# Performance work log

Measured on AMD Instinct MI355X. Metric: run time of the kernel, lower is better.

Reference implementation:

```python
import jax, jax.numpy as jnp
import numpy as np

T, K, N = 4096, 4096, 11008
EPS = 1e-5


def setup_inputs() -> dict:
    key = jax.random.key(0)
    k1, k2, k3, k4 = jax.random.split(key, 4)
    input_tensor = jax.random.normal(k1, (1, T, K), dtype=jnp.bfloat16)
    # int8 weights in [-127, 127]
    weight = jax.random.randint(k2, (N, K), -127, 128, dtype=jnp.int8)
    # per-output-channel weight scale, small positive values
    weight_scale = (jax.random.uniform(k3, (N, 1), dtype=jnp.float32) * 0.02 + 1e-4)
    bias = jax.random.normal(k4, (N,), dtype=jnp.bfloat16)
    return {"input_tensor": input_tensor, "weight": weight,
            "weight_scale": weight_scale, "bias": bias}


def _quantize_per_token_absmax(x):
    # x: [T, K] float -> int8 quant [T, K], float32 scale [T, 1]
    xf = x.astype(jnp.float32)
    absmax = jnp.max(jnp.abs(xf), axis=-1, keepdims=True)  # [T, 1]
    scale = jnp.maximum(absmax, EPS) / 127.0
    q = jnp.clip(jnp.round(xf / scale), -127, 127).astype(jnp.int8)
    return q, scale


def reference(input_tensor, weight, weight_scale, bias):
    x = jnp.squeeze(input_tensor, axis=0)                  # [T, K]
    x_q, x_scale = _quantize_per_token_absmax(x)           # int8 [T,K], f32 [T,1]
    # int8 GEMM with int32 accumulation: [T, K] @ [K, N]
    acc = jax.lax.dot_general(
        x_q, weight.T,
        dimension_numbers=(((1,), (0,)), ((), ())),
        preferred_element_type=jnp.int32,
    )
    # dequantize: per-token scale * per-channel scale
    out = (acc.astype(jnp.float32) * x_scale * weight_scale.T).astype(jnp.bfloat16)
    out = out + bias
    return out[None, :, :]                                  # [1, T, N]
```

## Files before the change

kernel.cpp:

```cpp
#include <hip/hip_runtime.h>
#include <hip/hip_bf16.h>
#include <stdint.h>

#define T_DIM 4096
#define K_DIM 4096
#define N_DIM 11008

#define XQ_OFF 0
#define XS_OFF 16777216
#define W8_OFF 16793600

typedef __attribute__((ext_vector_type(4))) int v4i;

__global__ __launch_bounds__(256) void prep_kernel(
    const float* __restrict__ x, int8_t* __restrict__ xq, float* __restrict__ xs,
    const int* __restrict__ w32, int8_t* __restrict__ w8)
{
    if (blockIdx.x < T_DIM / 4) {
        const int wid   = threadIdx.x >> 6;
        const int lane  = threadIdx.x & 63;
        const int token = blockIdx.x * 4 + wid;

        const float* xrow = x + (size_t)token * K_DIM;

        float4 v[16];
        float am = 0.0f;
#pragma unroll
        for (int j = 0; j < 16; ++j) {
            v[j] = *(const float4*)(xrow + (size_t)(j * 64 + lane) * 4);
            am = fmaxf(am, fmaxf(fmaxf(fabsf(v[j].x), fabsf(v[j].y)),
                                 fmaxf(fabsf(v[j].z), fabsf(v[j].w))));
        }
#pragma unroll
        for (int m = 1; m < 64; m <<= 1)
            am = fmaxf(am, __shfl_xor(am, m, 64));

        const float scale = fmaxf(am, 1e-5f) / 127.0f;
        if (lane == 0) xs[token] = scale;

        uint32_t* qrow = (uint32_t*)(xq + (size_t)token * K_DIM);
#pragma unroll
        for (int j = 0; j < 16; ++j) {
            int q0 = min(127, max(-127, (int)rintf(v[j].x / scale)));
            int q1 = min(127, max(-127, (int)rintf(v[j].y / scale)));
            int q2 = min(127, max(-127, (int)rintf(v[j].z / scale)));
            int q3 = min(127, max(-127, (int)rintf(v[j].w / scale)));
            qrow[j * 64 + lane] = ((uint32_t)(uint8_t)(int8_t)q0)       |
                                  ((uint32_t)(uint8_t)(int8_t)q1 << 8)  |
                                  ((uint32_t)(uint8_t)(int8_t)q2 << 16) |
                                  ((uint32_t)(uint8_t)(int8_t)q3 << 24);
        }
    } else {
        const size_t tid = (size_t)(blockIdx.x - T_DIM / 4) * 256 + threadIdx.x;
        const int4* src = (const int4*)w32 + tid * 4;
        uint32_t o[4];
#pragma unroll
        for (int i = 0; i < 4; ++i) {
            int4 a = src[i];
            o[i] = ((uint32_t)a.x & 0xFFu) | (((uint32_t)a.y & 0xFFu) << 8) |
                   (((uint32_t)a.z & 0xFFu) << 16) | ((uint32_t)a.w << 24);
        }
        *(uint4*)(w8 + tid * 16) = make_uint4(o[0], o[1], o[2], o[3]);
    }
}

#define BM 256
#define BN 256
#define BKB 128
#define NT (K_DIM / BKB)
#define MAT_SZ 32768

__global__ __launch_bounds__(512, 2) void gemm_i8_kernel(
    const int8_t* __restrict__ xq, const int8_t* __restrict__ w8,
    const float* __restrict__ xs, const float* __restrict__ wsc,
    const __hip_bfloat16* __restrict__ bias, float* __restrict__ out)
{
    __shared__ int8_t lds[2 * 2 * MAT_SZ];

    constexpr int NBN = N_DIM / BN;
    constexpr int NWG = (T_DIM / BM) * NBN;
    constexpr int CPX = NWG / 8;

    const int bid = blockIdx.x;
    const int b2  = (bid % 8) * CPX + bid / 8;
    const int bm  = b2 / NBN;
    const int bn  = b2 % NBN;

    const int tid  = threadIdx.x;
    const int wid  = tid >> 6;
    const int lane = tid & 63;
    const int wm   = wid >> 2;
    const int wn   = wid & 3;

    const int fr = lane & 15, kg = lane >> 4;
    int offA[8][2], offB[4][2];
#pragma unroll
    for (int mi = 0; mi < 8; ++mi) {
        const int row = wm * 128 + mi * 16 + fr;
#pragma unroll
        for (int ks = 0; ks < 2; ++ks)
            offA[mi][ks] = row * 128 + (((ks * 4 + kg) ^ (row & 7)) << 4);
    }
#pragma unroll
    for (int ni = 0; ni < 4; ++ni) {
        const int row = wn * 64 + ni * 16 + fr;
#pragma unroll
        for (int ks = 0; ks < 2; ++ks)
            offB[ni][ks] = row * 128 + (((ks * 4 + kg) ^ (row & 7)) << 4);
    }

    const int srow  = tid >> 3;
    const int sslot = tid & 7;
    const int csw   = (sslot ^ (srow & 7)) * 16;
    const int8_t* gA = xq + (size_t)(bm * BM + srow) * K_DIM + csw;
    const int8_t* gB = w8 + (size_t)(bn * BN + srow) * K_DIM + csw;
    const int ldsT = (tid & 511) * 16 - (lane * 16);
    const int ldsBase = (tid >> 6) * 1024;
    (void)ldsT;

    v4i acc[8][4];
#pragma unroll
    for (int mi = 0; mi < 8; ++mi)
#pragma unroll
        for (int ni = 0; ni < 4; ++ni) acc[mi][ni] = (v4i){0, 0, 0, 0};

#define STAGE(bufb, mat, r, kt)                                                 \
    __builtin_amdgcn_global_load_lds(                                           \
        (const __attribute__((address_space(1))) void*)(                        \
            ((mat) ? gB : gA) + (size_t)(r) * 64 * K_DIM + (size_t)(kt) * BKB), \
        (__attribute__((address_space(3))) void*)(                              \
            lds + ((bufb) * 2 + (mat)) * MAT_SZ + (r) * 8192 + ldsBase),        \
        16, 0, 0)

#define STAGE_TILE(bufb, kt)                                                    \
    do {                                                                        \
        STAGE(bufb, 0, 0, kt); STAGE(bufb, 0, 1, kt);                           \
        STAGE(bufb, 0, 2, kt); STAGE(bufb, 0, 3, kt);                           \
        STAGE(bufb, 1, 0, kt); STAGE(bufb, 1, 1, kt);                           \
        STAGE(bufb, 1, 2, kt); STAGE(bufb, 1, 3, kt);                           \
    } while (0)

    STAGE_TILE(0, 0);
    asm volatile("s_waitcnt vmcnt(0)" ::: "memory");
    __builtin_amdgcn_s_barrier();
    asm volatile("" ::: "memory");

    for (int t = 0; t < NT; ++t) {
        const int b  = t & 1;
        const int pn = b ^ 1;
        const int8_t* bA = lds + (b * 2 + 0) * MAT_SZ;
        const int8_t* bB = lds + (b * 2 + 1) * MAT_SZ;

        if (t + 1 < NT) STAGE_TILE(pn, t + 1);

#pragma unroll
        for (int ks = 0; ks < 2; ++ks) {
            v4i bF[4], aF[8];
#pragma unroll
            for (int ni = 0; ni < 4; ++ni)
                bF[ni] = *(const v4i*)(bB + offB[ni][ks]);
#pragma unroll
            for (int mi = 0; mi < 8; ++mi)
                aF[mi] = *(const v4i*)(bA + offA[mi][ks]);

            __builtin_amdgcn_s_setprio(1);
#pragma unroll
            for (int mi = 0; mi < 8; ++mi)
#pragma unroll
                for (int ni = 0; ni < 4; ++ni)
                    acc[mi][ni] = __builtin_amdgcn_mfma_i32_16x16x64_i8(
                        aF[mi], bF[ni], acc[mi][ni], 0, 0, 0);
            __builtin_amdgcn_s_setprio(0);
        }

        asm volatile("s_waitcnt vmcnt(0)" ::: "memory");
        __builtin_amdgcn_s_barrier();
        asm volatile("" ::: "memory");
    }

    const int row0 = bm * BM + wm * 128 + (lane >> 4) * 4;
    const int col0 = bn * BN + wn * 64 + (lane & 15);
#pragma unroll
    for (int mi = 0; mi < 8; ++mi) {
#pragma unroll
        for (int j = 0; j < 4; ++j) {
            const int row = row0 + mi * 16 + j;
            const float xscale = xs[row];
#pragma unroll
            for (int ni = 0; ni < 4; ++ni) {
                const int col = col0 + ni * 16;
                float p_  = (float)acc[mi][ni][j] * xscale * wsc[col];
                float pb_ = __bfloat162float(__float2bfloat16(p_));
                float vb  = __bfloat162float(__float2bfloat16(
                                pb_ + __bfloat162float(bias[col])));
                out[(size_t)row * N_DIM + col] = vb;
            }
        }
    }
#undef STAGE
#undef STAGE_TILE
}

extern "C" void kernel_launch(void* const* d_in, const int* in_sizes, int n_in,
                              void* d_out, int out_size, void* d_ws, size_t ws_size,
                              hipStream_t stream)
{
    const float*          x    = (const float*)d_in[0];
    const int*            w32  = (const int*)d_in[1];
    const float*          wsc  = (const float*)d_in[2];
    const __hip_bfloat16* bias = (const __hip_bfloat16*)d_in[3];
    float*                out  = (float*)d_out;

    int8_t* xq = (int8_t*)d_ws + XQ_OFF;
    float*  xs = (float*)((char*)d_ws + XS_OFF);
    int8_t* w8 = (int8_t*)d_ws + W8_OFF;

    prep_kernel<<<T_DIM / 4 + (N_DIM * (K_DIM / 16)) / 256, 256, 0, stream>>>(
        x, xq, xs, w32, w8);
    gemm_i8_kernel<<<(T_DIM / BM) * (N_DIM / BN), 512, 0, stream>>>(
        xq, w8, xs, wsc, bias, out);
}
```

Baseline: 258.0 us.

## Load weight fragments directly from global into registers, bypass LDS for B

Stops staging the weight tile through shared memory. Each wave instead reads its MFMA B fragments directly from global memory into double-buffered registers, while activations stay staged in LDS. This halves LDS footprint and removes the LDS reads for B. In exchange, B global traffic is duplicated across the wave rows, the loads are strided per row, and register pressure rises, which risks spills or reduced overlap.

```diff
diff --git a/kernel.cpp b/kernel.cpp
--- a/kernel.cpp
+++ b/kernel.cpp
@@ -68,14 +68,14 @@
 #define BN 256
 #define BKB 128
 #define NT (K_DIM / BKB)
-#define MAT_SZ 32768
+#define A_SZ 32768
 
 __global__ __launch_bounds__(512, 2) void gemm_i8_kernel(
     const int8_t* __restrict__ xq, const int8_t* __restrict__ w8,
     const float* __restrict__ xs, const float* __restrict__ wsc,
     const __hip_bfloat16* __restrict__ bias, float* __restrict__ out)
 {
-    __shared__ int8_t lds[2 * 2 * MAT_SZ];
+    __shared__ int8_t lds[2 * A_SZ];
 
     constexpr int NBN = N_DIM / BN;
     constexpr int NWG = (T_DIM / BM) * NBN;
@@ -93,7 +93,8 @@
     const int wn   = wid & 3;
 
     const int fr = lane & 15, kg = lane >> 4;
-    int offA[8][2], offB[4][2];
+
+    int offA[8][2];
 #pragma unroll
     for (int mi = 0; mi < 8; ++mi) {
         const int row = wm * 128 + mi * 16 + fr;
@@ -101,22 +102,17 @@
         for (int ks = 0; ks < 2; ++ks)
             offA[mi][ks] = row * 128 + (((ks * 4 + kg) ^ (row & 7)) << 4);
     }
-#pragma unroll
-    for (int ni = 0; ni < 4; ++ni) {
-        const int row = wn * 64 + ni * 16 + fr;
-#pragma unroll
-        for (int ks = 0; ks < 2; ++ks)
-            offB[ni][ks] = row * 128 + (((ks * 4 + kg) ^ (row & 7)) << 4);
-    }
+
+    const int8_t* gBf[4];
+#pragma unroll
+    for (int ni = 0; ni < 4; ++ni)
+        gBf[ni] = w8 + (size_t)(bn * BN + wn * 64 + ni * 16 + fr) * K_DIM + kg * 16;
 
     const int srow  = tid >> 3;
     const int sslot = tid & 7;
     const int csw   = (sslot ^ (srow & 7)) * 16;
     const int8_t* gA = xq + (size_t)(bm * BM + srow) * K_DIM + csw;
-    const int8_t* gB = w8 + (size_t)(bn * BN + srow) * K_DIM + csw;
-    const int ldsT = (tid & 511) * 16 - (lane * 16);
-    const int ldsBase = (tid >> 6) * 1024;
-    (void)ldsT;
+    const int ldsBase = wid * 1024;
 
     v4i acc[8][4];
 #pragma unroll
@@ -124,58 +120,62 @@
 #pragma unroll
         for (int ni = 0; ni < 4; ++ni) acc[mi][ni] = (v4i){0, 0, 0, 0};
 
-#define STAGE(bufb, mat, r, kt)                                                 \
-    __builtin_amdgcn_global_load_lds(                                           \
-        (const __attribute__((address_space(1))) void*)(                        \
-            ((mat) ? gB : gA) + (size_t)(r) * 64 * K_DIM + (size_t)(kt) * BKB), \
-        (__attribute__((address_space(3))) void*)(                              \
-            lds + ((bufb) * 2 + (mat)) * MAT_SZ + (r) * 8192 + ldsBase),        \
-        16, 0, 0)
-
-#define STAGE_TILE(bufb, kt)                                                    \
+#define STAGE_A(bufb, kt)                                                       \
     do {                                                                        \
-        STAGE(bufb, 0, 0, kt); STAGE(bufb, 0, 1, kt);                           \
-        STAGE(bufb, 0, 2, kt); STAGE(bufb, 0, 3, kt);                           \
-        STAGE(bufb, 1, 0, kt); STAGE(bufb, 1, 1, kt);                           \
-        STAGE(bufb, 1, 2, kt); STAGE(bufb, 1, 3, kt);                           \
+        _Pragma("unroll")                                                       \
+        for (int r = 0; r < 4; ++r)                                             \
+            __builtin_amdgcn_global_load_lds(                                   \
+                (const __attribute__((address_space(1))) void*)(                \
+                    gA + (size_t)r * 64 * K_DIM + (size_t)(kt) * BKB),          \
+                (__attribute__((address_space(3))) void*)(                      \
+                    lds + (bufb) * A_SZ + r * 8192 + ldsBase),                  \
+                16, 0, 0);                                                      \
     } while (0)
 
-    STAGE_TILE(0, 0);
+#define LOAD_B(dst, kt)                                                         \
+    do {                                                                        \
+        _Pragma("unroll")                                                       \
+        for (int ni = 0; ni < 4; ++ni) {                                        \
+            dst[ni][0] = *(const v4i*)(gBf[ni] + (size_t)(kt) * BKB);           \
+            dst[ni][1] = *(const v4i*)(gBf[ni] + (size_t)(kt) * BKB + 64);      \
+        }                                                                       \
+    } while (0)
+
+#define TILE_BODY(t, ab, BC, BNx)                                               \
+    do {                                                                        \
+        if ((t) + 1 < NT) { LOAD_B(BNx, (t) + 1); STAGE_A((ab) ^ 1, (t) + 1); } \
+        const int8_t* bA = lds + (ab) * A_SZ;                                   \
+        _Pragma("unroll")                                                       \
+        for (int ks = 0; ks < 2; ++ks) {                                        \
+            v4i aF[8];                                                          \
+            _Pragma("unroll")                                                   \
+            for (int mi = 0; mi < 8; ++mi)                                      \
+                aF[mi] = *(const v4i*)(bA + offA[mi][ks]);                      \
+            __builtin_amdgcn_s_setprio(1);                                      \
+            _Pragma("unroll")                                                   \
+            for (int mi = 0; mi < 8; ++mi)                                      \
+                _Pragma("unroll")                                               \
+                for (int ni = 0; ni < 4; ++ni)                                  \
+                    acc[mi][ni] = __builtin_amdgcn_mfma_i32_16x16x64_i8(        \
+                        aF[mi], BC[ni][ks], acc[mi][ni], 0, 0, 0);              \
+            __builtin_amdgcn_s_setprio(0);                                      \
+        }                                                                       \
+        asm volatile("s_waitcnt vmcnt(0)" ::: "memory");                        \
+        __builtin_amdgcn_s_barrier();                                           \
+        asm volatile("" ::: "memory");                                          \
+    } while (0)
+
+    v4i B0[4][2], B1[4][2];
+
+    LOAD_B(B0, 0);
+    STAGE_A(0, 0);
     asm volatile("s_waitcnt vmcnt(0)" ::: "memory");
     __builtin_amdgcn_s_barrier();
     asm volatile("" ::: "memory");
 
-    for (int t = 0; t < NT; ++t) {
-        const int b  = t & 1;
-        const int pn = b ^ 1;
-        const int8_t* bA = lds + (b * 2 + 0) * MAT_SZ;
-        const int8_t* bB = lds + (b * 2 + 1) * MAT_SZ;
-
-        if (t + 1 < NT) STAGE_TILE(pn, t + 1);
-
-#pragma unroll
-        for (int ks = 0; ks < 2; ++ks) {
-            v4i bF[4], aF[8];
-#pragma unroll
-            for (int ni = 0; ni < 4; ++ni)
-                bF[ni] = *(const v4i*)(bB + offB[ni][ks]);
-#pragma unroll
-            for (int mi = 0; mi < 8; ++mi)
-                aF[mi] = *(const v4i*)(bA + offA[mi][ks]);
-
-            __builtin_amdgcn_s_setprio(1);
-#pragma unroll
-            for (int mi = 0; mi < 8; ++mi)
-#pragma unroll
-                for (int ni = 0; ni < 4; ++ni)
-                    acc[mi][ni] = __builtin_amdgcn_mfma_i32_16x16x64_i8(
-                        aF[mi], bF[ni], acc[mi][ni], 0, 0, 0);
-            __builtin_amdgcn_s_setprio(0);
-        }
-
-        asm volatile("s_waitcnt vmcnt(0)" ::: "memory");
-        __builtin_amdgcn_s_barrier();
-        asm volatile("" ::: "memory");
+    for (int t = 0; t < NT; t += 2) {
+        TILE_BODY(t,     0, B0, B1);
+        TILE_BODY(t + 1, 1, B1, B0);
     }
 
     const int row0 = bm * BM + wm * 128 + (lane >> 4) * 4;
@@ -197,8 +197,9 @@
             }
         }
     }
-#undef STAGE
-#undef STAGE_TILE
+#undef STAGE_A
+#undef LOAD_B
+#undef TILE_BODY
 }
 
 extern "C" void kernel_launch(void* const* d_in, const int* in_sizes, int n_in,
```

Result: slower. 632.9 us (+145.3%).
